# Performance work log

Hardware: AMD Instinct MI355X
Metric: run time of the kernel (lower is better)

## Reference

```python
import jax, jax.numpy as jnp
import numpy as np


def setup_inputs() -> dict:
    key = jax.random.key(0)
    k1, k2 = jax.random.split(key)
    B, H, W = 16, 1024, 1024
    NB = 20
    preds = jax.random.randint(k1, (B, H, W), 0, NB, dtype=jnp.int32)
    targets = jax.random.randint(k2, (B, H, W), 0, NB, dtype=jnp.int32)
    return {"preds": preds, "targets": targets, "nb_class": NB, "smooth": 1}


def reference(preds, targets, nb_class, smooth):
    # Single-pass histogram formulation of the per-class IoU loop:
    #   intersection[c] = #{pred==c and target==c}
    #   union[c]        = #{pred==c} + #{target==c} - intersection[c]
    p = preds.reshape(-1)
    t = targets.reshape(-1)
    pred_count = jnp.bincount(p, length=nb_class).astype(jnp.float32)
    target_count = jnp.bincount(t, length=nb_class).astype(jnp.float32)
    # pixels where pred==target contribute to intersection of that class
    match = p == t
    intersection = jnp.bincount(jnp.where(match, p, nb_class), length=nb_class + 1)[:nb_class].astype(jnp.float32)
    union = pred_count + target_count - intersection
    s = jnp.float32(smooth)
    iou_per_class = (intersection + s) / (union + s)  # [nb_class]
    mIoU = iou_per_class.mean()
    return 1.0 - mIoU
```

## Files before the change

kernel.cpp:

```cpp
#include <hip/hip_runtime.h>
#include <hip/hip_bf16.h>


#define NB      20
#define NKEY    (NB * NB)
#define NCOPY   32
#define BLK     512
#define NSLOT   4
#define GRID_H  256
#define PSTRIDE 64

__device__ __forceinline__ void dma16(const void* g, void* l) {
    __builtin_amdgcn_global_load_lds(
        (const __attribute__((address_space(1))) unsigned*)g,
        (__attribute__((address_space(3))) unsigned*)l, 16, 0, 0);
}

__device__ __forceinline__ void process_pix(int p, int t, unsigned* hist_cp) {
    atomicAdd(&hist_cp[(p * NB + t) * NCOPY], 1u);
}

__device__ __forceinline__ void process_vec(int4 pv, int4 tv, unsigned* hist_cp) {
    process_pix(pv.x, tv.x, hist_cp);
    process_pix(pv.y, tv.y, hist_cp);
    process_pix(pv.z, tv.z, hist_cp);
    process_pix(pv.w, tv.w, hist_cp);
}

__global__ __launch_bounds__(BLK) void miou_hist_kernel(
        const int4* __restrict__ preds, const int4* __restrict__ targs,
        unsigned* __restrict__ partials, int n4, int full_iters) {
    __shared__ unsigned s_hist[NKEY * NCOPY];
    __shared__ int4 s_p[NSLOT][BLK];
    __shared__ int4 s_t[NSLOT][BLK];
    const int tid  = threadIdx.x;
    const int wid  = tid >> 6;
    const int lane = tid & 63;

    unsigned* hist_cp = &s_hist[tid & (NCOPY - 1)];
    const int CHUNK = gridDim.x * BLK;
    const int base  = blockIdx.x * BLK + tid;

    if (full_iters >= NSLOT) {
        #pragma unroll
        for (int s = 0; s < NSLOT; ++s) {
            dma16(&preds[base + s * CHUNK], &s_p[s][wid * 64]);
            dma16(&targs[base + s * CHUNK], &s_t[s][wid * 64]);
        }
    }
    for (int k = tid; k < NKEY * NCOPY; k += BLK) s_hist[k] = 0u;
    __syncthreads();

#define STEP(J, VM) do {                                              \
    const int slot_ = (J) & (NSLOT - 1);                              \
    asm volatile("s_waitcnt vmcnt(" #VM ")" ::: "memory");            \
    int4 pv_ = s_p[slot_][wid * 64 + lane];                           \
    int4 tv_ = s_t[slot_][wid * 64 + lane];                           \
    asm volatile("s_waitcnt lgkmcnt(0)" ::: "memory");                \
    if ((J) + NSLOT < full_iters) {                                   \
        dma16(&preds[base + ((J) + NSLOT) * CHUNK], &s_p[slot_][wid * 64]); \
        dma16(&targs[base + ((J) + NSLOT) * CHUNK], &s_t[slot_][wid * 64]); \
    }                                                                 \
    process_vec(pv_, tv_, hist_cp);                                   \
} while (0)

    if (full_iters >= NSLOT) {
        int j = 0;
        for (; j < full_iters - (NSLOT - 1); ++j) STEP(j, 6);
        STEP(j, 4); ++j;
        STEP(j, 2); ++j;
        STEP(j, 0);
    }
    for (int i = base + full_iters * CHUNK; i < n4; i += CHUNK) {
        int4 pv = preds[i];
        int4 tv = targs[i];
        process_vec(pv, tv, hist_cp);
    }
#undef STEP
    __syncthreads();

    unsigned* dst = &partials[(size_t)blockIdx.x * PSTRIDE];
    for (int c = wid; c < NB; c += (BLK / 64)) {
        unsigned pcs = 0;
        #pragma unroll
        for (int k = 0; k < 640; k += 64) pcs += s_hist[c * 640 + k + lane];

        unsigned tcs = 0;
        {
            const int copy = lane & 31;
            const int p0   = lane >> 5;
            #pragma unroll
            for (int p = 0; p < NB; p += 2)
                tcs += s_hist[((p + p0) * NB + c) * NCOPY + copy];
        }
        unsigned ics = (lane < NCOPY) ? s_hist[(c * 21) * NCOPY + lane] : 0u;

        #pragma unroll
        for (int off = 32; off > 0; off >>= 1) {
            pcs += __shfl_xor(pcs, off);
            tcs += __shfl_xor(tcs, off);
            ics += __shfl_xor(ics, off);
        }
        if (lane == 0) {
            dst[c]          = pcs;
            dst[NB + c]     = tcs;
            dst[2 * NB + c] = ics;
        }
    }
}

__global__ __launch_bounds__(1024) void miou_reduce_kernel(
        const unsigned* __restrict__ partials, int nblocks,
        const int* __restrict__ nb_ptr, const int* __restrict__ smooth_ptr,
        float* __restrict__ out) {
    __shared__ unsigned s_tot[PSTRIDE];
    if (threadIdx.x < PSTRIDE) s_tot[threadIdx.x] = 0u;
    __syncthreads();

    const int col4 = threadIdx.x & 15;
    const int seg  = threadIdx.x >> 4;
    const int4* p4 = (const int4*)partials;

    unsigned ax = 0, ay = 0, az = 0, aw = 0;
    #pragma unroll 8
    for (int r = seg; r < nblocks; r += 64) {
        int4 v = p4[r * 16 + col4];
        ax += (unsigned)v.x; ay += (unsigned)v.y;
        az += (unsigned)v.z; aw += (unsigned)v.w;
    }
    atomicAdd(&s_tot[col4 * 4 + 0], ax);
    atomicAdd(&s_tot[col4 * 4 + 1], ay);
    atomicAdd(&s_tot[col4 * 4 + 2], az);
    atomicAdd(&s_tot[col4 * 4 + 3], aw);
    __syncthreads();

    if (threadIdx.x == 0) {
        const int   nb = *nb_ptr;
        const float s  = (float)(*smooth_ptr);
        float acc_iou = 0.0f;
        for (int c = 0; c < nb && c < NB; ++c) {
            float pc    = (float)s_tot[c];
            float tc    = (float)s_tot[NB + c];
            float inter = (float)s_tot[2 * NB + c];
            float uni   = pc + tc - inter;
            acc_iou += (inter + s) / (uni + s);
        }
        out[0] = 1.0f - acc_iou / (float)nb;
    }
}

extern "C" void kernel_launch(void* const* d_in, const int* in_sizes, int n_in,
                              void* d_out, int out_size, void* d_ws, size_t ws_size,
                              hipStream_t stream) {
    const int4* preds      = (const int4*)d_in[0];
    const int4* targs      = (const int4*)d_in[1];
    const int*  nb_ptr     = (const int*)d_in[2];
    const int*  smooth_ptr = (const int*)d_in[3];
    float*      out        = (float*)d_out;

    int n  = in_sizes[0];
    int n4 = n >> 2;

    unsigned* partials = (unsigned*)d_ws;

    int grid = GRID_H;
    int max_grid = (n4 + BLK - 1) / BLK;
    if (grid > max_grid) grid = max_grid;
    size_t need_per_block = PSTRIDE * sizeof(unsigned);
    if ((size_t)grid * need_per_block > ws_size)
        grid = (int)(ws_size / need_per_block);

    int chunk = grid * BLK;
    int full  = (chunk > 0) ? (n4 / chunk) : 0;
    if (full < NSLOT) full = 0;

    miou_hist_kernel<<<grid, BLK, 0, stream>>>(preds, targs, partials, n4, full);
    miou_reduce_kernel<<<1, 1024, 0, stream>>>(partials, grid, nb_ptr, smooth_ptr, out);
}
```

Before: 30.87 us.

## Fuse final reduction into histogram kernel via last-block counter; deepen prefetch to six slots

Removes the separate reduce kernel launch. Each block bumps a global done counter after writing its partials, and the last block to finish sums all partials and computes the loss. The LDS prefetch ring grows from 4 to 6 slots with matching waitcnt values, so more global loads are in flight. This adds a hipMemsetAsync per call, and the larger LDS footprint may lower occupancy.

```diff
diff --git a/kernel.cpp b/kernel.cpp
--- a/kernel.cpp
+++ b/kernel.cpp
@@ -6,7 +6,7 @@
 #define NKEY    (NB * NB)
 #define NCOPY   32
 #define BLK     512
-#define NSLOT   4
+#define NSLOT   6
 #define GRID_H  256
 #define PSTRIDE 64
 
@@ -27,12 +27,15 @@
     process_pix(pv.w, tv.w, hist_cp);
 }
 
-__global__ __launch_bounds__(BLK) void miou_hist_kernel(
+__global__ __launch_bounds__(BLK) void miou_fused_kernel(
         const int4* __restrict__ preds, const int4* __restrict__ targs,
-        unsigned* __restrict__ partials, int n4, int full_iters) {
+        unsigned* __restrict__ partials, unsigned* __restrict__ done_ctr,
+        const int* __restrict__ nb_ptr, const int* __restrict__ smooth_ptr,
+        float* __restrict__ out, int n4, int full_iters) {
     __shared__ unsigned s_hist[NKEY * NCOPY];
     __shared__ int4 s_p[NSLOT][BLK];
     __shared__ int4 s_t[NSLOT][BLK];
+    __shared__ int s_last;
     const int tid  = threadIdx.x;
     const int wid  = tid >> 6;
     const int lane = tid & 63;
@@ -52,21 +55,26 @@
     __syncthreads();
 
 #define STEP(J, VM) do {                                              \
-    const int slot_ = (J) & (NSLOT - 1);                              \
+    const int slot_ = (J) & 7;   \
+    const int sl = (slot_ >= NSLOT) ? slot_ - NSLOT : slot_;          \
+    (void)sl;                                                         \
+    const int slot2_ = (J) % NSLOT;                                   \
     asm volatile("s_waitcnt vmcnt(" #VM ")" ::: "memory");            \
-    int4 pv_ = s_p[slot_][wid * 64 + lane];                           \
-    int4 tv_ = s_t[slot_][wid * 64 + lane];                           \
+    int4 pv_ = s_p[slot2_][wid * 64 + lane];                          \
+    int4 tv_ = s_t[slot2_][wid * 64 + lane];                          \
     asm volatile("s_waitcnt lgkmcnt(0)" ::: "memory");                \
     if ((J) + NSLOT < full_iters) {                                   \
-        dma16(&preds[base + ((J) + NSLOT) * CHUNK], &s_p[slot_][wid * 64]); \
-        dma16(&targs[base + ((J) + NSLOT) * CHUNK], &s_t[slot_][wid * 64]); \
+        dma16(&preds[base + ((J) + NSLOT) * CHUNK], &s_p[slot2_][wid * 64]); \
+        dma16(&targs[base + ((J) + NSLOT) * CHUNK], &s_t[slot2_][wid * 64]); \
     }                                                                 \
     process_vec(pv_, tv_, hist_cp);                                   \
 } while (0)
 
     if (full_iters >= NSLOT) {
         int j = 0;
-        for (; j < full_iters - (NSLOT - 1); ++j) STEP(j, 6);
+        for (; j < full_iters - (NSLOT - 1); ++j) STEP(j, 10);
+        STEP(j, 8); ++j;
+        STEP(j, 6); ++j;
         STEP(j, 4); ++j;
         STEP(j, 2); ++j;
         STEP(j, 0);
@@ -107,45 +115,45 @@
             dst[2 * NB + c] = ics;
         }
     }
-}
 
-__global__ __launch_bounds__(1024) void miou_reduce_kernel(
-        const unsigned* __restrict__ partials, int nblocks,
-        const int* __restrict__ nb_ptr, const int* __restrict__ smooth_ptr,
-        float* __restrict__ out) {
-    __shared__ unsigned s_tot[PSTRIDE];
-    if (threadIdx.x < PSTRIDE) s_tot[threadIdx.x] = 0u;
     __syncthreads();
-
-    const int col4 = threadIdx.x & 15;
-    const int seg  = threadIdx.x >> 4;
-    const int4* p4 = (const int4*)partials;
-
-    unsigned ax = 0, ay = 0, az = 0, aw = 0;
-    #pragma unroll 8
-    for (int r = seg; r < nblocks; r += 64) {
-        int4 v = p4[r * 16 + col4];
-        ax += (unsigned)v.x; ay += (unsigned)v.y;
-        az += (unsigned)v.z; aw += (unsigned)v.w;
+    if (tid == 0) {
+        __threadfence();
+        unsigned old = atomicAdd(done_ctr, 1u);
+        s_last = (old == gridDim.x - 1u) ? 1 : 0;
     }
-    atomicAdd(&s_tot[col4 * 4 + 0], ax);
-    atomicAdd(&s_tot[col4 * 4 + 1], ay);
-    atomicAdd(&s_tot[col4 * 4 + 2], az);
-    atomicAdd(&s_tot[col4 * 4 + 3], aw);
     __syncthreads();
-
-    if (threadIdx.x == 0) {
-        const int   nb = *nb_ptr;
-        const float s  = (float)(*smooth_ptr);
-        float acc_iou = 0.0f;
-        for (int c = 0; c < nb && c < NB; ++c) {
-            float pc    = (float)s_tot[c];
-            float tc    = (float)s_tot[NB + c];
-            float inter = (float)s_tot[2 * NB + c];
-            float uni   = pc + tc - inter;
-            acc_iou += (inter + s) / (uni + s);
+    if (s_last) {
+        __threadfence();
+        const int nblocks = gridDim.x;
+        const int col  = tid & 63;
+        const int rgrp = tid >> 6;
+        unsigned acc = 0;
+        for (int r = rgrp; r < nblocks; r += 8)
+            acc += partials[(size_t)r * PSTRIDE + col];
+        unsigned* red = (unsigned*)s_p;
+        red[rgrp * 64 + col] = acc;
+        __syncthreads();
+        if (tid < 64) {
+            unsigned tot = 0;
+            #pragma unroll
+            for (int k = 0; k < 8; ++k) tot += red[k * 64 + tid];
+            red[512 + tid] = tot;
         }
-        out[0] = 1.0f - acc_iou / (float)nb;
+        __syncthreads();
+        if (tid == 0) {
+            const int   nb = *nb_ptr;
+            const float s  = (float)(*smooth_ptr);
+            float acc_iou = 0.0f;
+            for (int c = 0; c < nb && c < NB; ++c) {
+                float pc    = (float)red[512 + c];
+                float tc    = (float)red[512 + NB + c];
+                float inter = (float)red[512 + 2 * NB + c];
+                float uni   = pc + tc - inter;
+                acc_iou += (inter + s) / (uni + s);
+            }
+            out[0] = 1.0f - acc_iou / (float)nb;
+        }
     }
 }
 
@@ -166,14 +174,18 @@
     int grid = GRID_H;
     int max_grid = (n4 + BLK - 1) / BLK;
     if (grid > max_grid) grid = max_grid;
+    if (grid < 1) grid = 1;
     size_t need_per_block = PSTRIDE * sizeof(unsigned);
-    if ((size_t)grid * need_per_block > ws_size)
-        grid = (int)(ws_size / need_per_block);
+    if ((size_t)(grid + 1) * need_per_block > ws_size)
+        grid = (int)(ws_size / need_per_block) - 1;
+
+    unsigned* done_ctr = partials + (size_t)grid * PSTRIDE;
+    hipMemsetAsync(done_ctr, 0, sizeof(unsigned), stream);
 
     int chunk = grid * BLK;
     int full  = (chunk > 0) ? (n4 / chunk) : 0;
     if (full < NSLOT) full = 0;
 
-    miou_hist_kernel<<<grid, BLK, 0, stream>>>(preds, targs, partials, n4, full);
-    miou_reduce_kernel<<<1, 1024, 0, stream>>>(partials, grid, nb_ptr, smooth_ptr, out);
+    miou_fused_kernel<<<grid, BLK, 0, stream>>>(
+        preds, targs, partials, done_ctr, nb_ptr, smooth_ptr, out, n4, full);
 }
```

Result: slower. 45.78 us (+48.3%).
